# Kernel tuning notes

Hardware: AMD Instinct MI355X
Metric: run time of the kernel (lower is better)

Reference implementation:

```python
import jax, jax.numpy as jnp
import numpy as np

B, C, H, W = 64, 8, 256, 256
CQ = C // 8  # = 1, required for torch.matmul broadcasting in the original


def setup_inputs() -> dict:
    key = jax.random.key(0)
    ks = jax.random.split(key, 7)
    x = jax.random.normal(ks[0], (B, C, H, W), jnp.float32)
    # 1x1 conv weights stored as [out_ch, in_ch] (kernel dims squeezed)
    w1 = jax.random.normal(ks[1], (CQ, C), jnp.float32) * (1.0 / np.sqrt(C))
    b1 = jax.random.normal(ks[2], (CQ,), jnp.float32) * 0.01
    w2 = jax.random.normal(ks[3], (CQ, C), jnp.float32) * (1.0 / np.sqrt(C))
    b2 = jax.random.normal(ks[4], (CQ,), jnp.float32) * 0.01
    w3 = jax.random.normal(ks[5], (C, C), jnp.float32) * (1.0 / np.sqrt(C))
    b3 = jax.random.normal(ks[6], (C,), jnp.float32) * 0.01
    return {"x": x, "w1": w1, "b1": b1, "w2": w2, "b2": b2, "w3": w3, "b3": b3}


def reference(x, w1, b1, w2, b2, w3, b3):
    # 1x1 convs == channel contractions
    q = jnp.einsum('bchw,oc->bohw', x, w1) + b1[None, :, None, None]  # [B,1,H,W]
    k = jnp.einsum('bchw,oc->bohw', x, w2) + b2[None, :, None, None]  # [B,1,H,W]
    v = jnp.einsum('bchw,oc->bohw', x, w3) + b3[None, :, None, None]  # [B,C,H,W]
    # scores[b,i,j] = sum_w q[b,0,i,w] * k[b,0,j,w]   (q @ k^T over dims 2,3)
    scores = jnp.einsum('bhw,bgw->bhg', q[:, 0], k[:, 0])  # [B,H,H]
    attn = jax.nn.softmax(scores, axis=-1)
    # out[b,c,i,w] = sum_j attn[b,i,j] * v[b,c,j,w]  (broadcast over C)
    out = jnp.einsum('bhg,bcgw->bchw', attn, v)  # [B,C,H,W]
    return out
```

## Files before the change

kernel.cpp:

```cpp
#include <hip/hip_runtime.h>

typedef _Float16 h16;
typedef __attribute__((ext_vector_type(2))) _Float16 half2v;
typedef __attribute__((ext_vector_type(4))) _Float16 half4;
typedef __attribute__((ext_vector_type(8))) _Float16 half8;
typedef __attribute__((ext_vector_type(4))) float f32x4;

#define Cn 8
#define HWn 65536
#define CHWn 524288

#define PADW 42
__global__ __launch_bounds__(256) void prep_kernel(
    const float* __restrict__ x, const float* __restrict__ w1, const float* __restrict__ b1,
    const float* __restrict__ w2, const float* __restrict__ b2,
    const float* __restrict__ w3, const float* __restrict__ b3,
    h16* __restrict__ qh, h16* __restrict__ kh, h16* __restrict__ vt) {
  const int wt = blockIdx.x, jt = blockIdx.y, b = blockIdx.z;
  const int j0 = jt * 32, w0 = wt * 32;
  const int t = threadIdx.x;
  const int jl = t >> 3, wq = t & 7;
  __shared__ h16 sv[8 * 32 * PADW];

  float4 xv[8];
  const float* xb = x + ((size_t)b << 19) + (size_t)(j0 + jl) * 256 + w0 + wq * 4;
#pragma unroll
  for (int ci = 0; ci < 8; ci++)
    xv[ci] = *(const float4*)(xb + ((size_t)ci << 16));

  float qa[4], ka[4], va[8][4];
  const float bb1 = b1[0], bb2 = b2[0];
#pragma unroll
  for (int e = 0; e < 4; e++) { qa[e] = bb1; ka[e] = bb2; }
#pragma unroll
  for (int co = 0; co < 8; co++) {
    const float bv = b3[co];
#pragma unroll
    for (int e = 0; e < 4; e++) va[co][e] = bv;
  }
#pragma unroll
  for (int ci = 0; ci < 8; ci++) {
    const float xe[4] = {xv[ci].x, xv[ci].y, xv[ci].z, xv[ci].w};
    const float w1c = w1[ci], w2c = w2[ci];
#pragma unroll
    for (int e = 0; e < 4; e++) {
      qa[e] = fmaf(xe[e], w1c, qa[e]);
      ka[e] = fmaf(xe[e], w2c, ka[e]);
    }
#pragma unroll
    for (int co = 0; co < 8; co++) {
      const float w3c = w3[co * 8 + ci];
#pragma unroll
      for (int e = 0; e < 4; e++) va[co][e] = fmaf(xe[e], w3c, va[co][e]);
    }
  }

  {
    half4 qv = {(h16)qa[0], (h16)qa[1], (h16)qa[2], (h16)qa[3]};
    half4 kv = {(h16)ka[0], (h16)ka[1], (h16)ka[2], (h16)ka[3]};
    size_t off = ((size_t)b << 16) + (size_t)(j0 + jl) * 256 + w0 + wq * 4;
    *(half4*)&qh[off] = qv;
    *(half4*)&kh[off] = kv;
  }

#pragma unroll
  for (int co = 0; co < 8; co++) {
    half2v v01 = {(h16)va[co][0], (h16)va[co][1]};
    half2v v23 = {(h16)va[co][2], (h16)va[co][3]};
    h16* p = &sv[co * 32 * PADW + jl * PADW + wq * 4];
    *(half2v*)p = v01;
    *(half2v*)(p + 2) = v23;
  }
  __syncthreads();

#pragma unroll
  for (int cc = 0; cc < 4; cc++) {
    const int cid = t + 256 * cc;
    const int co = cid >> 7;
    const int w = (cid >> 2) & 31;
    const int jc = cid & 3;
    const h16* rp = &sv[co * 32 * PADW + (jc * 8) * PADW + w];
    half8 pk;
#pragma unroll
    for (int e = 0; e < 8; e++) pk[e] = rp[e * PADW];
    *(half8*)&vt[((size_t)(b * Cn + co) * 256 + w0 + w) * 256 + j0 + jc * 8] = pk;
  }
}

__global__ __launch_bounds__(256) void scores_kernel(
    const h16* __restrict__ qh, const h16* __restrict__ kh, h16* __restrict__ p) {
  const int i0 = blockIdx.x * 16, b = blockIdx.y;
  const int t = threadIdx.x, wv = t >> 6, lane = t & 63;
  const int m = lane & 15, quad = lane >> 4;
  __shared__ float red[2][4][16];
  const h16* qrow = qh + ((size_t)b << 16) + (size_t)(i0 + m) * 256 + quad * 8;
  const h16* kbase = kh + ((size_t)b << 16) + (size_t)(wv * 64 + m) * 256 + quad * 8;
  f32x4 acc[4];
#pragma unroll
  for (int jt = 0; jt < 4; jt++) acc[jt] = {0.f, 0.f, 0.f, 0.f};
#pragma unroll
  for (int s = 0; s < 8; s++) {
    half8 Q = *(const half8*)(qrow + s * 32);
#pragma unroll
    for (int jt = 0; jt < 4; jt++) {
      half8 K = *(const half8*)(kbase + (size_t)jt * 4096 + s * 32);
      acc[jt] = __builtin_amdgcn_mfma_f32_16x16x32_f16(K, Q, acc[jt], 0, 0, 0);
    }
  }
  float mx = -3.4e38f;
#pragma unroll
  for (int jt = 0; jt < 4; jt++)
#pragma unroll
    for (int r = 0; r < 4; r++) mx = fmaxf(mx, acc[jt][r]);
  mx = fmaxf(mx, __shfl_xor(mx, 16, 64));
  mx = fmaxf(mx, __shfl_xor(mx, 32, 64));
  if (lane < 16) red[0][wv][lane] = mx;
  __syncthreads();
  float gmx = fmaxf(fmaxf(red[0][0][m], red[0][1][m]), fmaxf(red[0][2][m], red[0][3][m]));
  float sum = 0.f;
#pragma unroll
  for (int jt = 0; jt < 4; jt++)
#pragma unroll
    for (int r = 0; r < 4; r++) {
      float e = __expf(acc[jt][r] - gmx);
      acc[jt][r] = e;
      sum += e;
    }
  sum += __shfl_xor(sum, 16, 64);
  sum += __shfl_xor(sum, 32, 64);
  if (lane < 16) red[1][wv][lane] = sum;
  __syncthreads();
  const float inv = 1.f / (red[1][0][m] + red[1][1][m] + red[1][2][m] + red[1][3][m]);
  h16* pb = p + ((size_t)b << 16) + (size_t)(i0 + m) * 256;
#pragma unroll
  for (int jt = 0; jt < 4; jt++) {
    half4 pv = {(h16)(acc[jt][0] * inv), (h16)(acc[jt][1] * inv),
                (h16)(acc[jt][2] * inv), (h16)(acc[jt][3] * inv)};
    *(half4*)&pb[wv * 64 + jt * 16 + quad * 4] = pv;
  }
}

__global__ __launch_bounds__(256) void apply_kernel_mfma(
    const h16* __restrict__ p, const h16* __restrict__ vt, float* __restrict__ out) {
  const int bx = blockIdx.x, b = blockIdx.y;
  const int it = bx >> 4, nt = bx & 15;
  const int i0 = it * 128, n0 = nt * 128;
  const int t = threadIdx.x, wv = t >> 6, lane = t & 63;
  const int m = lane & 15, quad = lane >> 4;
  const int wy = wv >> 1, wx = wv & 1;
  __shared__ h16 As[128 * 40];
  __shared__ h16 Bs[128 * 40];
  const int srow = t >> 2, soff = (t & 3) * 8;
  const h16* gA = p + ((size_t)b << 16) + (size_t)(i0 + srow) * 256 + soff;
  const h16* gB = vt + (size_t)(b * 2048 + n0 + srow) * 256 + soff;
  uint4 ra0 = *(const uint4*)gA;
  uint4 ra1 = *(const uint4*)(gA + 64 * 256);
  uint4 rb0 = *(const uint4*)gB;
  uint4 rb1 = *(const uint4*)(gB + 64 * 256);
  f32x4 acc[4][4];
#pragma unroll
  for (int ai = 0; ai < 4; ai++)
#pragma unroll
    for (int bi = 0; bi < 4; bi++) acc[ai][bi] = {0.f, 0.f, 0.f, 0.f};
  const int lA = srow * 40 + soff;
  for (int kc = 0; kc < 8; kc++) {
    __syncthreads();
    *(uint4*)&As[lA] = ra0; *(uint4*)&As[lA + 64 * 40] = ra1;
    *(uint4*)&Bs[lA] = rb0; *(uint4*)&Bs[lA + 64 * 40] = rb1;
    __syncthreads();
    if (kc < 7) {
      const int ko = (kc + 1) * 32;
      ra0 = *(const uint4*)(gA + ko);
      ra1 = *(const uint4*)(gA + 64 * 256 + ko);
      rb0 = *(const uint4*)(gB + ko);
      rb1 = *(const uint4*)(gB + 64 * 256 + ko);
    }
    half8 af[4], bf[4];
#pragma unroll
    for (int ai = 0; ai < 4; ai++)
      af[ai] = *(const half8*)&As[(wy * 64 + ai * 16 + m) * 40 + quad * 8];
#pragma unroll
    for (int bi = 0; bi < 4; bi++)
      bf[bi] = *(const half8*)&Bs[(wx * 64 + bi * 16 + m) * 40 + quad * 8];
#pragma unroll
    for (int ai = 0; ai < 4; ai++)
#pragma unroll
      for (int bi = 0; bi < 4; bi++)
        acc[ai][bi] = __builtin_amdgcn_mfma_f32_16x16x32_f16(af[ai], bf[bi], acc[ai][bi], 0, 0, 0);
  }
  const int c = nt >> 1;
  const int wcol0 = (nt & 1) * 128 + wx * 64;
  float* ob = out + ((size_t)(b * Cn + c) << 16);
#pragma unroll
  for (int ai = 0; ai < 4; ai++) {
    const int ib = i0 + wy * 64 + ai * 16 + quad * 4;
#pragma unroll
    for (int r = 0; r < 4; r++)
#pragma unroll
      for (int bi = 0; bi < 4; bi++)
        ob[(size_t)(ib + r) * 256 + wcol0 + bi * 16 + m] = acc[ai][bi][r];
  }
}

__global__ __launch_bounds__(256) void qk_kernel(
    const float* __restrict__ x, const float* __restrict__ w1, const float* __restrict__ b1,
    const float* __restrict__ w2, const float* __restrict__ b2,
    float* __restrict__ q, float* __restrict__ k) {
  int n = blockIdx.x * 256 + threadIdx.x;
  int b = n >> 16;
  int pidx = n & 65535;
  const float* xb = x + (size_t)b * CHWn + pidx;
  float qa = b1[0], ka = b2[0];
#pragma unroll
  for (int c = 0; c < Cn; c++) {
    float xv = xb[c * HWn];
    qa = fmaf(xv, w1[c], qa);
    ka = fmaf(xv, w2[c], ka);
  }
  q[n] = qa;
  k[n] = ka;
}

__global__ __launch_bounds__(256) void scores_kernel_f32(
    const float* __restrict__ q, const float* __restrict__ k, float* __restrict__ sc) {
  const int jt = blockIdx.x, it = blockIdx.y, b = blockIdx.z;
  const int i0 = it * 128, j0 = jt * 128;
  const int t = threadIdx.x;
  const int tx = t & 15, ty = t >> 4;
  __shared__ __align__(16) float qt[32 * 132];
  __shared__ __align__(16) float kt[32 * 132];
  float acc[2][2][4][4];
#pragma unroll
  for (int a = 0; a < 2; a++)
#pragma unroll
    for (int bb = 0; bb < 2; bb++)
#pragma unroll
      for (int il = 0; il < 4; il++)
#pragma unroll
        for (int jl = 0; jl < 4; jl++) acc[a][bb][il][jl] = 0.f;
  const float* qb = q + (size_t)b * HWn;
  const float* kb = k + (size_t)b * HWn;
  for (int kc = 0; kc < 8; kc++) {
    const int w0 = kc * 32;
    __syncthreads();
#pragma unroll
    for (int e = 0; e < 16; e++) {
      int idx = t + 256 * e;
      int r = idx >> 5, c = idx & 31;
      qt[c * 132 + r] = qb[(i0 + r) * 256 + w0 + c];
      kt[c * 132 + r] = kb[(j0 + r) * 256 + w0 + c];
    }
    __syncthreads();
#pragma unroll 4
    for (int w = 0; w < 32; w++) {
      const float4 a0 = *(const float4*)&qt[w * 132 + ty * 4];
      const float4 a1 = *(const float4*)&qt[w * 132 + 64 + ty * 4];
      const float4 b0 = *(const float4*)&kt[w * 132 + tx * 4];
      const float4 b1 = *(const float4*)&kt[w * 132 + 64 + tx * 4];
      const float av[2][4] = {{a0.x, a0.y, a0.z, a0.w}, {a1.x, a1.y, a1.z, a1.w}};
      const float bv[2][4] = {{b0.x, b0.y, b0.z, b0.w}, {b1.x, b1.y, b1.z, b1.w}};
#pragma unroll
      for (int ih = 0; ih < 2; ih++)
#pragma unroll
        for (int jh = 0; jh < 2; jh++)
#pragma unroll
          for (int il = 0; il < 4; il++)
#pragma unroll
            for (int jl = 0; jl < 4; jl++)
              acc[ih][jh][il][jl] = fmaf(av[ih][il], bv[jh][jl], acc[ih][jh][il][jl]);
    }
  }
  float* scb = sc + (size_t)b * HWn;
#pragma unroll
  for (int ih = 0; ih < 2; ih++)
#pragma unroll
    for (int il = 0; il < 4; il++) {
      int i = i0 + ih * 64 + ty * 4 + il;
#pragma unroll
      for (int jh = 0; jh < 2; jh++) {
        float4 st = make_float4(acc[ih][jh][il][0], acc[ih][jh][il][1],
                                acc[ih][jh][il][2], acc[ih][jh][il][3]);
        *(float4*)&scb[i * 256 + j0 + jh * 64 + tx * 4] = st;
      }
    }
}

__global__ __launch_bounds__(256) void softmax_kernel(float* __restrict__ at) {
  int wave = (blockIdx.x * 256 + threadIdx.x) >> 6;
  int lane = threadIdx.x & 63;
  float* row = at + (size_t)wave * 256;
  float v[4];
  float mm = -3.4e38f;
#pragma unroll
  for (int u = 0; u < 4; u++) {
    v[u] = row[lane + 64 * u];
    mm = fmaxf(mm, v[u]);
  }
#pragma unroll
  for (int o = 1; o < 64; o <<= 1) mm = fmaxf(mm, __shfl_xor(mm, o, 64));
  float s = 0.f;
#pragma unroll
  for (int u = 0; u < 4; u++) {
    v[u] = __expf(v[u] - mm);
    s += v[u];
  }
#pragma unroll
  for (int o = 1; o < 64; o <<= 1) s += __shfl_xor(s, o, 64);
  float inv = 1.0f / s;
#pragma unroll
  for (int u = 0; u < 4; u++) row[lane + 64 * u] = v[u] * inv;
}

__global__ __launch_bounds__(256, 2) void apply_kernel(
    const float* __restrict__ x, const float* __restrict__ at,
    const float* __restrict__ w3, const float* __restrict__ b3, float* __restrict__ out) {
  const int it = blockIdx.x, b = blockIdx.y;
  const int i0 = it * 16;
  const int t = threadIdx.x;
  __shared__ __align__(16) float pt[16 * 256];
  const float* atb = at + (size_t)b * HWn + i0 * 256;
#pragma unroll
  for (int e = 0; e < 4; e++)
    *(float4*)&pt[t * 4 + 1024 * e] = *(const float4*)&atb[t * 4 + 1024 * e];
  __syncthreads();
  float acc[8][16];
#pragma unroll
  for (int c = 0; c < 8; c++)
#pragma unroll
    for (int ii = 0; ii < 16; ii++) acc[c][ii] = 0.f;
  const float* xb = x + (size_t)b * CHWn + t;
  for (int j0 = 0; j0 < 256; j0 += 2) {
    float p2[16][2];
#pragma unroll
    for (int ii = 0; ii < 16; ii++) {
      float2 pp = *(const float2*)&pt[ii * 256 + j0];
      p2[ii][0] = pp.x;
      p2[ii][1] = pp.y;
    }
#pragma unroll
    for (int ju = 0; ju < 2; ju++) {
      float xv[8];
#pragma unroll
      for (int c = 0; c < 8; c++) xv[c] = xb[c * HWn + (j0 + ju) * 256];
#pragma unroll
      for (int c = 0; c < 8; c++)
#pragma unroll
        for (int ii = 0; ii < 16; ii++)
          acc[c][ii] = fmaf(xv[c], p2[ii][ju], acc[c][ii]);
    }
  }
#pragma unroll
  for (int co = 0; co < 8; co++) {
    float wr[8];
#pragma unroll
    for (int ci = 0; ci < 8; ci++) wr[ci] = w3[co * 8 + ci];
    float bb = b3[co];
#pragma unroll
    for (int ii = 0; ii < 16; ii++) {
      float o = bb;
#pragma unroll
      for (int ci = 0; ci < 8; ci++) o = fmaf(wr[ci], acc[ci][ii], o);
      out[(size_t)b * CHWn + co * HWn + (i0 + ii) * 256 + t] = o;
    }
  }
}

extern "C" void kernel_launch(void* const* d_in, const int* in_sizes, int n_in,
                              void* d_out, int out_size, void* d_ws, size_t ws_size,
                              hipStream_t stream) {
  const float* x  = (const float*)d_in[0];
  const float* w1 = (const float*)d_in[1];
  const float* b1 = (const float*)d_in[2];
  const float* w2 = (const float*)d_in[3];
  const float* b2 = (const float*)d_in[4];
  const float* w3 = (const float*)d_in[5];
  const float* b3 = (const float*)d_in[6];
  float* out = (float*)d_out;

  if (ws_size >= (size_t)92274688) {
    char* wsb = (char*)d_ws;
    h16* vt = (h16*)wsb;
    h16* qh = (h16*)(wsb + 67108864);
    h16* kh = (h16*)(wsb + 75497472);
    h16* p  = (h16*)(wsb + 83886080);
    prep_kernel<<<dim3(8, 8, 64), dim3(256), 0, stream>>>(x, w1, b1, w2, b2, w3, b3, qh, kh, vt);
    scores_kernel<<<dim3(16, 64), dim3(256), 0, stream>>>(qh, kh, p);
    apply_kernel_mfma<<<dim3(32, 64), dim3(256), 0, stream>>>(p, vt, out);
  } else {
    float* wsf = (float*)d_ws;
    float* q  = wsf;
    float* k  = wsf + 4194304;
    float* at = wsf + 8388608;
    qk_kernel<<<dim3(16384), dim3(256), 0, stream>>>(x, w1, b1, w2, b2, q, k);
    scores_kernel_f32<<<dim3(2, 2, 64), dim3(256), 0, stream>>>(q, k, at);
    softmax_kernel<<<dim3(4096), dim3(256), 0, stream>>>(at);
    apply_kernel<<<dim3(16, 64), dim3(256), 0, stream>>>(x, at, w3, b3, out);
  }
}
```

Measured before the change: 308.3 us.

## Fuse scores/softmax and attention-apply into one kernel keeping P in LDS

Replaces the separate scores+softmax kernel and the attention-apply GEMM with a single fused kernel. Each 512-thread block computes a 64-row tile of scores, normalises it, stores the probabilities in shared memory, preloads them as MFMA A fragments, then streams all V columns from global memory to produce the output. This removes the write and reread of the fp16 probability matrix and one launch. In exchange the grid shrinks to 256 blocks, V is read directly from global memory without LDS staging (each block rereads all of V for its batch), and register pressure is high from holding 32 half8 fragments.

```diff
diff --git a/kernel.cpp b/kernel.cpp
--- a/kernel.cpp
+++ b/kernel.cpp
@@ -87,39 +87,43 @@
   }
 }
 
-__global__ __launch_bounds__(256) void scores_kernel(
-    const h16* __restrict__ qh, const h16* __restrict__ kh, h16* __restrict__ p) {
-  const int i0 = blockIdx.x * 16, b = blockIdx.y;
+__global__ __launch_bounds__(512, 2) void fused_sa(
+    const h16* __restrict__ qh, const h16* __restrict__ kh,
+    const h16* __restrict__ vt, float* __restrict__ out) {
+  const int it = blockIdx.x, b = blockIdx.y;
   const int t = threadIdx.x, wv = t >> 6, lane = t & 63;
   const int m = lane & 15, quad = lane >> 4;
-  __shared__ float red[2][4][16];
-  const h16* qrow = qh + ((size_t)b << 16) + (size_t)(i0 + m) * 256 + quad * 8;
-  const h16* kbase = kh + ((size_t)b << 16) + (size_t)(wv * 64 + m) * 256 + quad * 8;
-  f32x4 acc[4];
-#pragma unroll
-  for (int jt = 0; jt < 4; jt++) acc[jt] = {0.f, 0.f, 0.f, 0.f};
+  const int iw = wv >> 1, jw = wv & 1;
+  __shared__ h16 Ps[64 * 264];
+  __shared__ float red[2][8][16];
+
+  const h16* qrow = qh + ((size_t)b << 16) + (size_t)(it * 64 + iw * 16 + m) * 256 + quad * 8;
+  const h16* kbase = kh + ((size_t)b << 16) + (size_t)(jw * 128 + m) * 256 + quad * 8;
+  f32x4 acc[8];
+#pragma unroll
+  for (int jt = 0; jt < 8; jt++) acc[jt] = {0.f, 0.f, 0.f, 0.f};
 #pragma unroll
   for (int s = 0; s < 8; s++) {
     half8 Q = *(const half8*)(qrow + s * 32);
 #pragma unroll
-    for (int jt = 0; jt < 4; jt++) {
-      half8 K = *(const half8*)(kbase + (size_t)jt * 4096 + s * 32);
+    for (int jt = 0; jt < 8; jt++) {
+      half8 K = *(const half8*)(kbase + jt * 4096 + s * 32);
       acc[jt] = __builtin_amdgcn_mfma_f32_16x16x32_f16(K, Q, acc[jt], 0, 0, 0);
     }
   }
   float mx = -3.4e38f;
 #pragma unroll
-  for (int jt = 0; jt < 4; jt++)
+  for (int jt = 0; jt < 8; jt++)
 #pragma unroll
     for (int r = 0; r < 4; r++) mx = fmaxf(mx, acc[jt][r]);
   mx = fmaxf(mx, __shfl_xor(mx, 16, 64));
   mx = fmaxf(mx, __shfl_xor(mx, 32, 64));
   if (lane < 16) red[0][wv][lane] = mx;
   __syncthreads();
-  float gmx = fmaxf(fmaxf(red[0][0][m], red[0][1][m]), fmaxf(red[0][2][m], red[0][3][m]));
+  const float gmx = fmaxf(red[0][iw * 2][m], red[0][iw * 2 + 1][m]);
   float sum = 0.f;
 #pragma unroll
-  for (int jt = 0; jt < 4; jt++)
+  for (int jt = 0; jt < 8; jt++)
 #pragma unroll
     for (int r = 0; r < 4; r++) {
       float e = __expf(acc[jt][r] - gmx);
@@ -130,75 +134,42 @@
   sum += __shfl_xor(sum, 32, 64);
   if (lane < 16) red[1][wv][lane] = sum;
   __syncthreads();
-  const float inv = 1.f / (red[1][0][m] + red[1][1][m] + red[1][2][m] + red[1][3][m]);
-  h16* pb = p + ((size_t)b << 16) + (size_t)(i0 + m) * 256;
-#pragma unroll
-  for (int jt = 0; jt < 4; jt++) {
+  const float inv = 1.f / (red[1][iw * 2][m] + red[1][iw * 2 + 1][m]);
+#pragma unroll
+  for (int jt = 0; jt < 8; jt++) {
     half4 pv = {(h16)(acc[jt][0] * inv), (h16)(acc[jt][1] * inv),
                 (h16)(acc[jt][2] * inv), (h16)(acc[jt][3] * inv)};
-    *(half4*)&pb[wv * 64 + jt * 16 + quad * 4] = pv;
-  }
-}
-
-__global__ __launch_bounds__(256) void apply_kernel_mfma(
-    const h16* __restrict__ p, const h16* __restrict__ vt, float* __restrict__ out) {
-  const int bx = blockIdx.x, b = blockIdx.y;
-  const int it = bx >> 4, nt = bx & 15;
-  const int i0 = it * 128, n0 = nt * 128;
-  const int t = threadIdx.x, wv = t >> 6, lane = t & 63;
-  const int m = lane & 15, quad = lane >> 4;
-  const int wy = wv >> 1, wx = wv & 1;
-  __shared__ h16 As[128 * 40];
-  __shared__ h16 Bs[128 * 40];
-  const int srow = t >> 2, soff = (t & 3) * 8;
-  const h16* gA = p + ((size_t)b << 16) + (size_t)(i0 + srow) * 256 + soff;
-  const h16* gB = vt + (size_t)(b * 2048 + n0 + srow) * 256 + soff;
-  uint4 ra0 = *(const uint4*)gA;
-  uint4 ra1 = *(const uint4*)(gA + 64 * 256);
-  uint4 rb0 = *(const uint4*)gB;
-  uint4 rb1 = *(const uint4*)(gB + 64 * 256);
-  f32x4 acc[4][4];
-#pragma unroll
-  for (int ai = 0; ai < 4; ai++)
-#pragma unroll
-    for (int bi = 0; bi < 4; bi++) acc[ai][bi] = {0.f, 0.f, 0.f, 0.f};
-  const int lA = srow * 40 + soff;
-  for (int kc = 0; kc < 8; kc++) {
-    __syncthreads();
-    *(uint4*)&As[lA] = ra0; *(uint4*)&As[lA + 64 * 40] = ra1;
-    *(uint4*)&Bs[lA] = rb0; *(uint4*)&Bs[lA + 64 * 40] = rb1;
-    __syncthreads();
-    if (kc < 7) {
-      const int ko = (kc + 1) * 32;
-      ra0 = *(const uint4*)(gA + ko);
-      ra1 = *(const uint4*)(gA + 64 * 256 + ko);
-      rb0 = *(const uint4*)(gB + ko);
-      rb1 = *(const uint4*)(gB + 64 * 256 + ko);
-    }
-    half8 af[4], bf[4];
+    *(half4*)&Ps[(iw * 16 + m) * 264 + jw * 128 + jt * 16 + quad * 4] = pv;
+  }
+  __syncthreads();
+
+  half8 afr[8][4];
+#pragma unroll
+  for (int kc = 0; kc < 8; kc++)
 #pragma unroll
     for (int ai = 0; ai < 4; ai++)
-      af[ai] = *(const half8*)&As[(wy * 64 + ai * 16 + m) * 40 + quad * 8];
-#pragma unroll
-    for (int bi = 0; bi < 4; bi++)
-      bf[bi] = *(const half8*)&Bs[(wx * 64 + bi * 16 + m) * 40 + quad * 8];
+      afr[kc][ai] = *(const half8*)&Ps[(ai * 16 + m) * 264 + kc * 32 + quad * 8];
+
+  for (int nt = 0; nt < 16; nt++) {
+    const int c = nt >> 1;
+    const int wloc = (nt & 1) * 128 + wv * 16 + m;
+    const h16* vrow = vt + ((size_t)((b * 8 + c) * 256 + wloc) << 8) + quad * 8;
+    f32x4 a2[4];
+#pragma unroll
+    for (int ai = 0; ai < 4; ai++) a2[ai] = {0.f, 0.f, 0.f, 0.f};
+#pragma unroll
+    for (int kc = 0; kc < 8; kc++) {
+      half8 bf = *(const half8*)(vrow + kc * 32);
+#pragma unroll
+      for (int ai = 0; ai < 4; ai++)
+        a2[ai] = __builtin_amdgcn_mfma_f32_16x16x32_f16(afr[kc][ai], bf, a2[ai], 0, 0, 0);
+    }
+    float* ob = out + (((size_t)(b * 8 + c)) << 16) + (size_t)(it * 64 + quad * 4) * 256 + wloc;
 #pragma unroll
     for (int ai = 0; ai < 4; ai++)
 #pragma unroll
-      for (int bi = 0; bi < 4; bi++)
-        acc[ai][bi] = __builtin_amdgcn_mfma_f32_16x16x32_f16(af[ai], bf[bi], acc[ai][bi], 0, 0, 0);
-  }
-  const int c = nt >> 1;
-  const int wcol0 = (nt & 1) * 128 + wx * 64;
-  float* ob = out + ((size_t)(b * Cn + c) << 16);
-#pragma unroll
-  for (int ai = 0; ai < 4; ai++) {
-    const int ib = i0 + wy * 64 + ai * 16 + quad * 4;
-#pragma unroll
-    for (int r = 0; r < 4; r++)
-#pragma unroll
-      for (int bi = 0; bi < 4; bi++)
-        ob[(size_t)(ib + r) * 256 + wcol0 + bi * 16 + m] = acc[ai][bi][r];
+      for (int r = 0; r < 4; r++)
+        ob[(size_t)(ai * 16 + r) * 256] = a2[ai][r];
   }
 }
 
@@ -382,10 +353,8 @@
     h16* vt = (h16*)wsb;
     h16* qh = (h16*)(wsb + 67108864);
     h16* kh = (h16*)(wsb + 75497472);
-    h16* p  = (h16*)(wsb + 83886080);
     prep_kernel<<<dim3(8, 8, 64), dim3(256), 0, stream>>>(x, w1, b1, w2, b2, w3, b3, qh, kh, vt);
-    scores_kernel<<<dim3(16, 64), dim3(256), 0, stream>>>(qh, kh, p);
-    apply_kernel_mfma<<<dim3(32, 64), dim3(256), 0, stream>>>(p, vt, out);
+    fused_sa<<<dim3(4, 64), dim3(512), 0, stream>>>(qh, kh, vt, out);
   } else {
     float* wsf = (float*)d_ws;
     float* q  = wsf;
```

Result: slower. 352.0 us (+14.2%).

## Restructure apply GEMM to stage full-K V tile in LDS and stream P

Applied to the files above, without the earlier changes.

The apply kernel now uses 512-thread blocks, each covering all 256 output rows for a 64-column slice of one channel. The whole 64x256 V tile is loaded into LDS once, and the P fragments are read directly from global memory into MFMA operands. This removes the per-k-step double-barrier staging of both operands. In exchange, every block rereads the full P matrix for its batch from global memory or cache, and each wave works on a smaller 64x32 sub-tile.

```diff
diff --git a/kernel.cpp b/kernel.cpp
--- a/kernel.cpp
+++ b/kernel.cpp
@@ -140,65 +140,56 @@
   }
 }
 
-__global__ __launch_bounds__(256) void apply_kernel_mfma(
+__global__ __launch_bounds__(512, 4) void apply_kernel_v2(
     const h16* __restrict__ p, const h16* __restrict__ vt, float* __restrict__ out) {
-  const int bx = blockIdx.x, b = blockIdx.y;
-  const int it = bx >> 4, nt = bx & 15;
-  const int i0 = it * 128, n0 = nt * 128;
+  const int nb = blockIdx.x, b = blockIdx.y;
+  const int c = nb >> 2, w0 = (nb & 3) * 64;
   const int t = threadIdx.x, wv = t >> 6, lane = t & 63;
   const int m = lane & 15, quad = lane >> 4;
-  const int wy = wv >> 1, wx = wv & 1;
-  __shared__ h16 As[128 * 40];
-  __shared__ h16 Bs[128 * 40];
-  const int srow = t >> 2, soff = (t & 3) * 8;
-  const h16* gA = p + ((size_t)b << 16) + (size_t)(i0 + srow) * 256 + soff;
-  const h16* gB = vt + (size_t)(b * 2048 + n0 + srow) * 256 + soff;
-  uint4 ra0 = *(const uint4*)gA;
-  uint4 ra1 = *(const uint4*)(gA + 64 * 256);
-  uint4 rb0 = *(const uint4*)gB;
-  uint4 rb1 = *(const uint4*)(gB + 64 * 256);
-  f32x4 acc[4][4];
+  const int iw = wv >> 1, nw = wv & 1;
+  __shared__ h16 Bs[64 * 264];
+
+  const h16* vbase = vt + (((size_t)(b * Cn + c) * 256 + w0) << 8);
+#pragma unroll
+  for (int e = 0; e < 4; e++) {
+    const int idx = t + 512 * e;
+    const int row = idx >> 5, ch = idx & 31;
+    *(uint4*)&Bs[row * 264 + ch * 8] = *(const uint4*)&vbase[(size_t)row * 256 + ch * 8];
+  }
+  __syncthreads();
+
+  const h16* gA = p + ((size_t)b << 16) + (size_t)(iw * 64 + m) * 256 + quad * 8;
+  f32x4 acc[4][2];
 #pragma unroll
   for (int ai = 0; ai < 4; ai++)
 #pragma unroll
-    for (int bi = 0; bi < 4; bi++) acc[ai][bi] = {0.f, 0.f, 0.f, 0.f};
-  const int lA = srow * 40 + soff;
+    for (int bi = 0; bi < 2; bi++) acc[ai][bi] = {0.f, 0.f, 0.f, 0.f};
+
+#pragma unroll
   for (int kc = 0; kc < 8; kc++) {
-    __syncthreads();
-    *(uint4*)&As[lA] = ra0; *(uint4*)&As[lA + 64 * 40] = ra1;
-    *(uint4*)&Bs[lA] = rb0; *(uint4*)&Bs[lA + 64 * 40] = rb1;
-    __syncthreads();
-    if (kc < 7) {
-      const int ko = (kc + 1) * 32;
-      ra0 = *(const uint4*)(gA + ko);
-      ra1 = *(const uint4*)(gA + 64 * 256 + ko);
-      rb0 = *(const uint4*)(gB + ko);
-      rb1 = *(const uint4*)(gB + 64 * 256 + ko);
-    }
-    half8 af[4], bf[4];
+    half8 af[4], bf[2];
 #pragma unroll
     for (int ai = 0; ai < 4; ai++)
-      af[ai] = *(const half8*)&As[(wy * 64 + ai * 16 + m) * 40 + quad * 8];
-#pragma unroll
-    for (int bi = 0; bi < 4; bi++)
-      bf[bi] = *(const half8*)&Bs[(wx * 64 + bi * 16 + m) * 40 + quad * 8];
+      af[ai] = *(const half8*)(gA + (size_t)ai * 4096 + kc * 32);
+#pragma unroll
+    for (int bi = 0; bi < 2; bi++)
+      bf[bi] = *(const half8*)&Bs[(nw * 32 + bi * 16 + m) * 264 + kc * 32 + quad * 8];
 #pragma unroll
     for (int ai = 0; ai < 4; ai++)
 #pragma unroll
-      for (int bi = 0; bi < 4; bi++)
+      for (int bi = 0; bi < 2; bi++)
         acc[ai][bi] = __builtin_amdgcn_mfma_f32_16x16x32_f16(af[ai], bf[bi], acc[ai][bi], 0, 0, 0);
   }
-  const int c = nt >> 1;
-  const int wcol0 = (nt & 1) * 128 + wx * 64;
-  float* ob = out + ((size_t)(b * Cn + c) << 16);
+
+  float* ob = out + (((size_t)(b * Cn + c)) << 16) + w0 + nw * 32;
 #pragma unroll
   for (int ai = 0; ai < 4; ai++) {
-    const int ib = i0 + wy * 64 + ai * 16 + quad * 4;
+    const int ib = iw * 64 + ai * 16 + quad * 4;
 #pragma unroll
     for (int r = 0; r < 4; r++)
 #pragma unroll
-      for (int bi = 0; bi < 4; bi++)
-        ob[(size_t)(ib + r) * 256 + wcol0 + bi * 16 + m] = acc[ai][bi][r];
+      for (int bi = 0; bi < 2; bi++)
+        ob[(size_t)(ib + r) * 256 + bi * 16 + m] = acc[ai][bi][r];
   }
 }
 
@@ -385,7 +376,7 @@
     h16* p  = (h16*)(wsb + 83886080);
     prep_kernel<<<dim3(8, 8, 64), dim3(256), 0, stream>>>(x, w1, b1, w2, b2, w3, b3, qh, kh, vt);
     scores_kernel<<<dim3(16, 64), dim3(256), 0, stream>>>(qh, kh, p);
-    apply_kernel_mfma<<<dim3(32, 64), dim3(256), 0, stream>>>(p, vt, out);
+    apply_kernel_v2<<<dim3(32, 64), dim3(512), 0, stream>>>(p, vt, out);
   } else {
     float* wsf = (float*)d_ws;
     float* q  = wsf;
```

After: 338.9 us. +9.9%, slower.
